# Optimization experiments

Hardware: AMD Instinct MI355X
Metric: run time of the kernel (lower is better)

Reference implementation:

```python
import jax, jax.numpy as jnp
import numpy as np
import math

B, T, D, DI, DFF, H = 4, 1024, 1024, 256, 4096, 16
S, N, E = 16, 256, 1024          # stat_num, token_num, exemplar_len
STAT_K, TOKEN_K = 8, 16
NEG = -1e6


def setup_inputs() -> dict:
    key = jax.random.key(0)
    ks = jax.random.split(key, 32)
    r = lambda i, shape: jax.random.normal(ks[i], shape, jnp.float32)
    w = lambda i, shape: r(i, shape) * 0.02
    return dict(
        x=r(0, (B, T, D)),
        stat_enc=r(1, (B * S, N, D)),
        exemplar_enc=r(2, (B, E, D)),
        stat_feature=r(3, (B, S, D)),
        intent_embed=r(4, (B, 1, DI)),
        Wq1=w(5, (D, D)), Wk1=w(6, (D, D)), Wv1=w(7, (D, D)), Wo1=w(8, (D, D)),
        Wq_stat=w(9, (D + DI, D)), Wq_token=w(10, (D + DI, D)),
        Wk_stat=w(11, (D, D)), Wk_token=w(12, (D, D)),
        Wv_sel=w(13, (D, D)), Wo_sel=w(14, (D, D)),
        Wq2=w(15, (D + DI, D)), Wk2=w(16, (D, D)), Wv2=w(17, (D, D)), Wo2=w(18, (D, D)),
        Wg=w(19, (2 * D, 1)),
        W1=w(20, (D, DFF)), b1=jnp.zeros((DFF,), jnp.float32),
        W2=w(21, (DFF, D)), b2=jnp.zeros((D,), jnp.float32),
        g1=jnp.ones((D,), jnp.float32), be1=jnp.zeros((D,), jnp.float32),
        g2=jnp.ones((D,), jnp.float32), be2=jnp.zeros((D,), jnp.float32),
        g3=jnp.ones((D,), jnp.float32), be3=jnp.zeros((D,), jnp.float32),
        stat_valid_len=jax.random.randint(ks[22], (B,), 1, S + 1),
        example_valid_len=jax.random.randint(ks[23], (B,), 1, E + 1),
    )


def _ln(x, g, b):
    m = x.mean(-1, keepdims=True)
    v = ((x - m) ** 2).mean(-1, keepdims=True)
    return (x - m) / jnp.sqrt(v + 1e-5) * g + b


def _mha(q, k, v, valid, Wq, Wk, Wv, Wo):
    Bq, Tq, _ = q.shape
    Sk = k.shape[1]
    sp = lambda z: z.reshape(Bq, z.shape[1], H, -1).transpose(0, 2, 1, 3)  # B,H,L,dh
    qh, kh, vh = sp(q @ Wq), sp(k @ Wk), sp(v @ Wv)
    dh = qh.shape[-1]
    sc = jnp.einsum('bhtd,bhsd->bhts', qh, kh) / math.sqrt(dh)
    vl = valid[:, None, None, None] if valid.ndim == 1 else valid[:, None, :, None]
    sc = jnp.where(jnp.arange(Sk)[None, None, None, :] < vl, sc, NEG)
    w = jax.nn.softmax(sc, axis=-1)
    out = jnp.einsum('bhts,bhsd->bhtd', w, vh).transpose(0, 2, 1, 3).reshape(Bq, Tq, -1)
    return out @ Wo


def _scatter_topk(scores, k):
    # keep top-k per row, everything else -> NEG (matches torch topk+scatter)
    shp = scores.shape
    flat = scores.reshape(-1, shp[-1])
    vals, idx = jax.lax.top_k(flat, k)
    out = jnp.full_like(flat, NEG).at[jnp.arange(flat.shape[0])[:, None], idx].set(vals)
    return out.reshape(shp)


def reference(x, stat_enc, exemplar_enc, stat_feature, intent_embed,
              Wq1, Wk1, Wv1, Wo1,
              Wq_stat, Wq_token, Wk_stat, Wk_token, Wv_sel, Wo_sel,
              Wq2, Wk2, Wv2, Wo2, Wg,
              W1, b1, W2, b2,
              g1, be1, g2, be2, g3, be3,
              stat_valid_len, example_valid_len):
    # masked self-attention (training mode -> causal valid lens)
    dec_valid = jnp.broadcast_to(jnp.arange(1, T + 1)[None, :], (B, T))
    x2 = _mha(x, x, x, dec_valid, Wq1, Wk1, Wv1, Wo1)
    y = _ln(x + x2, g1, be1)
    yi = jnp.concatenate([y, jnp.broadcast_to(intent_embed, (B, T, DI))], axis=-1)

    # selective hierarchical top-k attention
    qs = yi @ Wq_stat                      # [B,T,D]
    qt = yi @ Wq_token                     # [B,T,D]
    ks = stat_feature @ Wk_stat            # [B,S,D]
    kt = (stat_enc @ Wk_token).reshape(B, S, N, D)
    vv = (stat_enc @ Wv_sel).reshape(B, S, N, D)
    scale = math.sqrt(D)
    ssc = jnp.einsum('btd,bsd->bts', qs, ks) / scale
    ssc = jnp.where(jnp.arange(S)[None, None, :] < stat_valid_len[:, None, None], ssc, NEG)
    sw = jax.nn.softmax(_scatter_topk(ssc, min(S - 1, STAT_K)), axis=-1)   # [B,T,S]
    tsc = jnp.einsum('btd,bsnd->btsn', qt, kt) / scale                      # [B,T,S,N]
    tw = jax.nn.softmax(_scatter_topk(tsc, min(N - 1, TOKEN_K)), axis=-1)
    comb = sw[..., None] * tw                                               # [B,T,S,N]
    y2s = jnp.einsum('btsn,bsnd->btd', comb, vv) @ Wo_sel

    # exemplar cross-attention
    y2e = _mha(yi, exemplar_enc, exemplar_enc, example_valid_len, Wq2, Wk2, Wv2, Wo2)

    gate = jax.nn.sigmoid(jnp.concatenate([y2s, y2e], axis=-1) @ Wg)
    y2 = gate * y2s + (1.0 - gate) * y2e
    z = _ln(y + 2.0 * y2, g2, be2)
    ffn = jax.nn.relu(z @ W1 + b1) @ W2 + b2
    return _ln(z + ffn, g3, be3)
```

## Files before the change

kernel.cpp:

```cpp
#include <hip/hip_runtime.h>

typedef unsigned short u16;
typedef short s16x8 __attribute__((ext_vector_type(8)));
typedef u16 u16x4 __attribute__((ext_vector_type(4)));
typedef float f32x4 __attribute__((ext_vector_type(4)));

#define T_N   1024
#define NEGV  -1e6f
#define MB    (1L << 20)

__device__ __forceinline__ u16 f2bf(float f) {
    unsigned u = __float_as_uint(f);
    u += 0x7fffu + ((u >> 16) & 1u);
    return (u16)(u >> 16);
}
__device__ __forceinline__ float bf2f(u16 h) {
    return __uint_as_float(((unsigned)h) << 16);
}
__device__ __forceinline__ f32x4 mfma16(s16x8 a, s16x8 b, f32x4 c) {
    return __builtin_amdgcn_mfma_f32_16x16x32_bf16(a, b, c, 0, 0, 0);
}
__device__ __forceinline__ void gll16(const u16* g, u16* l) {
    __builtin_amdgcn_global_load_lds((const __attribute__((address_space(1))) void*)g,
                                     (__attribute__((address_space(3))) void*)l, 16, 0, 0);
}

struct P6 { const float* s[6]; u16* d[6]; };

__global__ __launch_bounds__(256) void transpose_cast_batch(P6 pp, int K, int N) {
    const float* __restrict__ src = pp.s[blockIdx.z];
    u16* __restrict__ dst = pp.d[blockIdx.z];
    __shared__ float tile[32][33];
    int nb = blockIdx.x * 32, kb = blockIdx.y * 32;
    int tx = threadIdx.x & 31, ty = threadIdx.x >> 5;
    #pragma unroll
    for (int i = 0; i < 4; i++)
        tile[ty + 8*i][tx] = src[(long)(kb + ty + 8*i) * N + nb + tx];
    __syncthreads();
    #pragma unroll
    for (int i = 0; i < 4; i++)
        dst[(long)(nb + ty + 8*i) * K + kb + tx] = f2bf(tile[tx][ty + 8*i]);
}

__global__ __launch_bounds__(256) void cast_bf16_kernel(const float* __restrict__ src,
                                                        u16* __restrict__ dst, long n) {
    long i = ((long)blockIdx.x * 256 + threadIdx.x) * 4;
    if (i >= n) return;
    float4 v = *(const float4*)(src + i);
    u16x4 o = { f2bf(v.x), f2bf(v.y), f2bf(v.z), f2bf(v.w) };
    *(u16x4*)(dst + i) = o;
}

template<typename OutT, bool RELU, bool HAS_BIAS>
__global__ __launch_bounds__(256) void gemm_bt(
    const u16* __restrict__ A, const u16* __restrict__ Bt, OutT* __restrict__ C,
    const float* __restrict__ bias, int M, int N, int K,
    int lda, int ldb, int ldc,
    int batchDivA, long sA, long sB, long sC)
{
    A  += (long)(blockIdx.z / batchDivA) * sA;
    Bt += (long)blockIdx.z * sB;
    C  += (long)blockIdx.z * sC;
    __shared__ __align__(16) u16 As[4096];
    __shared__ __align__(16) u16 Bs[4096];
    const int tid = threadIdx.x;
    const int wave = tid >> 6, lane = tid & 63;
    const int quad = lane >> 4, l16 = lane & 15;
    const int wr = (wave >> 1) * 64, wc = (wave & 1) * 64;
    const long row0 = (long)blockIdx.y * 128, col0 = (long)blockIdx.x * 128;

    f32x4 acc[4][4] = {};

    const int l4r = lane >> 2;
    const int l4c = (lane & 3) * 8;
    const int ra = wave * 32 + l4r;
    const u16* Ap0 = A + (row0 + ra) * (long)lda + l4c;
    const u16* Ap1 = Ap0 + 16L * lda;
    const u16* Bp0 = Bt + (col0 + ra) * (long)ldb + l4c;
    const u16* Bp1 = Bp0 + 16L * ldb;
    u16* AsW0 = &As[(wave * 32) * 32];
    u16* AsW1 = &As[(wave * 32 + 16) * 32];
    u16* BsW0 = &Bs[(wave * 32) * 32];
    u16* BsW1 = &Bs[(wave * 32 + 16) * 32];
    const bool aok0 = (row0 + wave * 32) < M;
    const bool aok1 = (row0 + wave * 32 + 16) < M;

    for (int k0 = 0; k0 < K; k0 += 32) {
        __syncthreads();
        if (aok0) gll16(Ap0 + k0, AsW0);
        if (aok1) gll16(Ap1 + k0, AsW1);
        gll16(Bp0 + k0, BsW0);
        gll16(Bp1 + k0, BsW1);
        __syncthreads();
        s16x8 af[4], bfr[4];
        #pragma unroll
        for (int i = 0; i < 4; i++)
            af[i]  = *(const s16x8*)&As[(wr + i*16 + l16) * 32 + quad*8];
        #pragma unroll
        for (int j = 0; j < 4; j++)
            bfr[j] = *(const s16x8*)&Bs[(wc + j*16 + l16) * 32 + quad*8];
        #pragma unroll
        for (int i = 0; i < 4; i++)
            #pragma unroll
            for (int j = 0; j < 4; j++)
                acc[i][j] = mfma16(af[i], bfr[j], acc[i][j]);
    }

    #pragma unroll
    for (int i = 0; i < 4; i++) {
        long row = row0 + wr + i*16 + quad*4;
        #pragma unroll
        for (int j = 0; j < 4; j++) {
            long col = col0 + wc + j*16 + l16;
            float bv = 0.f;
            if constexpr (HAS_BIAS) bv = bias[col];
            #pragma unroll
            for (int r = 0; r < 4; r++) {
                if (row + r < M) {
                    float v = acc[i][j][r] + bv;
                    if constexpr (RELU) v = fmaxf(v, 0.f);
                    if constexpr (sizeof(OutT) == 2) C[(row + r) * (long)ldc + col] = f2bf(v);
                    else                             C[(row + r) * (long)ldc + col] = v;
                }
            }
        }
    }
}

template<bool CAUSAL>
__global__ __launch_bounds__(256) void flash_attn_kernel(
    const u16* __restrict__ Q, const u16* __restrict__ Kg, const u16* __restrict__ Vg,
    const int* __restrict__ valid_len, u16* __restrict__ O,
    int qld, int kld, int vld)
{
    const int h = blockIdx.y, b = blockIdx.z;
    const int qt0 = blockIdx.x * 64;
    const int tid = threadIdx.x;
    const int wave = tid >> 6, lane = tid & 63;
    const int quad = lane >> 4, l16 = lane & 15;

    __shared__ __align__(16) u16 Qs[64][72];
    __shared__ __align__(16) u16 Ks[64][72];
    __shared__ __align__(16) u16 Vt[64][72];
    __shared__ __align__(16) u16 Ps[4][16][72];

    const int sr = tid >> 2, scc = (tid & 3) * 16;
    {
        const u16* qp = Q + ((long)b * T_N + qt0 + sr) * qld + h * 64 + scc;
        *(s16x8*)&Qs[sr][scc]     = *(const s16x8*)qp;
        *(s16x8*)&Qs[sr][scc + 8] = *(const s16x8*)(qp + 8);
    }
    float m_i[4] = {-1e30f, -1e30f, -1e30f, -1e30f};
    float l_i[4] = {0.f, 0.f, 0.f, 0.f};
    f32x4 o_acc[4] = {};

    int vl = 0, kend;
    if (CAUSAL) kend = qt0 + 64;
    else { vl = valid_len[b]; kend = (vl + 63) & ~63; }

    for (int kv0 = 0; kv0 < kend; kv0 += 64) {
        __syncthreads();
        {
            const u16* kp = Kg + ((long)b * T_N + kv0 + sr) * kld + h * 64 + scc;
            *(s16x8*)&Ks[sr][scc]     = *(const s16x8*)kp;
            *(s16x8*)&Ks[sr][scc + 8] = *(const s16x8*)(kp + 8);
            const u16* vp = Vg + ((long)b * T_N + kv0 + sr) * vld + h * 64 + scc;
            s16x8 v0 = *(const s16x8*)vp;
            s16x8 v1 = *(const s16x8*)(vp + 8);
            #pragma unroll
            for (int j = 0; j < 8; j++) {
                Vt[scc + j][sr]     = (u16)v0[j];
                Vt[scc + 8 + j][sr] = (u16)v1[j];
            }
        }
        __syncthreads();
        f32x4 sc[4] = {};
        #pragma unroll
        for (int kk = 0; kk < 64; kk += 32) {
            s16x8 aq = *(const s16x8*)&Qs[wave*16 + l16][kk + quad*8];
            #pragma unroll
            for (int j = 0; j < 4; j++) {
                s16x8 bk = *(const s16x8*)&Ks[j*16 + l16][kk + quad*8];
                sc[j] = mfma16(aq, bk, sc[j]);
            }
        }
        const int qrow = qt0 + wave*16 + quad*4;
        #pragma unroll
        for (int j = 0; j < 4; j++) {
            int kcol = kv0 + j*16 + l16;
            #pragma unroll
            for (int r = 0; r < 4; r++) {
                float s = sc[j][r] * 0.125f;
                bool ok = CAUSAL ? (kcol <= qrow + r) : (kcol < vl);
                sc[j][r] = ok ? s : -1e30f;
            }
        }
        float alpha[4];
        #pragma unroll
        for (int r = 0; r < 4; r++) {
            float mx = fmaxf(fmaxf(sc[0][r], sc[1][r]), fmaxf(sc[2][r], sc[3][r]));
            #pragma unroll
            for (int d = 1; d < 16; d <<= 1) mx = fmaxf(mx, __shfl_xor(mx, d, 64));
            float mn = fmaxf(m_i[r], mx);
            alpha[r] = __expf(m_i[r] - mn);
            m_i[r] = mn;
        }
        float rsum[4] = {0.f, 0.f, 0.f, 0.f};
        #pragma unroll
        for (int j = 0; j < 4; j++)
            #pragma unroll
            for (int r = 0; r < 4; r++) {
                float pv = __expf(sc[j][r] - m_i[r]);
                sc[j][r] = pv;
                rsum[r] += pv;
            }
        #pragma unroll
        for (int r = 0; r < 4; r++) {
            #pragma unroll
            for (int d = 1; d < 16; d <<= 1) rsum[r] += __shfl_xor(rsum[r], d, 64);
            l_i[r] = l_i[r] * alpha[r] + rsum[r];
        }
        #pragma unroll
        for (int j = 0; j < 4; j++)
            #pragma unroll
            for (int r = 0; r < 4; r++)
                Ps[wave][quad*4 + r][j*16 + l16] = f2bf(sc[j][r]);
        #pragma unroll
        for (int j2 = 0; j2 < 4; j2++)
            #pragma unroll
            for (int r = 0; r < 4; r++)
                o_acc[j2][r] *= alpha[r];
        __syncthreads();
        #pragma unroll
        for (int kk = 0; kk < 64; kk += 32) {
            s16x8 ap = *(const s16x8*)&Ps[wave][l16][kk + quad*8];
            #pragma unroll
            for (int j2 = 0; j2 < 4; j2++) {
                s16x8 bv = *(const s16x8*)&Vt[j2*16 + l16][kk + quad*8];
                o_acc[j2] = mfma16(ap, bv, o_acc[j2]);
            }
        }
    }
    #pragma unroll
    for (int j2 = 0; j2 < 4; j2++) {
        #pragma unroll
        for (int r = 0; r < 4; r++) {
            float v = o_acc[j2][r] / l_i[r];
            long row = (long)b * T_N + qt0 + wave*16 + quad*4 + r;
            O[row * 1024 + h*64 + j2*16 + l16] = f2bf(v);
        }
    }
}

__global__ __launch_bounds__(256) void ssc_kernel(
    const u16* __restrict__ qs, const u16* __restrict__ ks,
    const int* __restrict__ svl, float* __restrict__ ssc, int qld)
{
    const int t = blockIdx.x, b = blockIdx.y;
    const int wave = threadIdx.x >> 6, lane = threadIdx.x & 63;
    const u16* qrow = qs + ((long)b * T_N + t) * qld + lane * 16;
    const int vl = svl[b];
    for (int s = wave; s < 16; s += 4) {
        const u16* krow = ks + ((long)b * 16 + s) * 1024 + lane * 16;
        float acc = 0.f;
        #pragma unroll
        for (int seg = 0; seg < 2; seg++) {
            s16x8 qv = *(const s16x8*)(qrow + seg*8);
            s16x8 kv = *(const s16x8*)(krow + seg*8);
            #pragma unroll
            for (int j = 0; j < 8; j++) acc += bf2f((u16)qv[j]) * bf2f((u16)kv[j]);
        }
        #pragma unroll
        for (int d = 1; d < 64; d <<= 1) acc += __shfl_xor(acc, d, 64);
        if (lane == 0)
            ssc[((long)b * T_N + t) * 16 + s] = (s < vl) ? acc * (1.f/32.f) : NEGV;
    }
}

__global__ __launch_bounds__(256) void select_combine_kernel(
    const float* __restrict__ ssc, const float* __restrict__ tsc,
    const u16* __restrict__ vv, u16* __restrict__ out, int t0, int vld)
{
    const int tl = blockIdx.x, b = blockIdx.y;
    const int tg = t0 + tl;
    const int tid = threadIdx.x;
    const int wave = tid >> 6, lane = tid & 63;
    __shared__ float coeff[128];
    __shared__ long  rowoff[128];
    __shared__ int   sel_s[8];
    __shared__ float sel_w[8];

    if (wave == 0) {
        float cur = (lane < 16) ? ssc[((long)b * T_N + tg) * 16 + lane] : -3e38f;
        float mx0 = 0.f, ssum = 0.f, myv = -3e38f;
        int myi = 0;
        #pragma unroll
        for (int it = 0; it < 8; it++) {
            float mv = cur; int mi = lane;
            #pragma unroll
            for (int d = 1; d < 64; d <<= 1) {
                float ov = __shfl_xor(mv, d, 64);
                int   oi = __shfl_xor(mi, d, 64);
                if (ov > mv || (ov == mv && oi < mi)) { mv = ov; mi = oi; }
            }
            if (it == 0) mx0 = mv;
            ssum += __expf(mv - mx0);
            if (lane == it) { myv = mv; myi = mi; }
            if (lane == mi) cur = -3e38f;
        }
        if (lane < 8) { sel_s[lane] = myi; sel_w[lane] = __expf(myv - mx0) / ssum; }
    }
    __syncthreads();

    for (int slot = wave; slot < 8; slot += 4) {
        int s = sel_s[slot];
        float sw = sel_w[slot];
        const float* trow = tsc + (((long)b * 16 + s) * 512 + tl) * 256;
        float4 lv4 = *(const float4*)(trow + lane * 4);
        float loc[4] = { lv4.x, lv4.y, lv4.z, lv4.w };
        float mx0 = 0.f, tsum = 0.f, myv = -3e38f;
        int myi = 0;
        for (int it = 0; it < 16; it++) {
            float mv = -3e38f; int mi = 0;
            #pragma unroll
            for (int u = 0; u < 4; u++)
                if (loc[u] > mv) { mv = loc[u]; mi = lane*4 + u; }
            #pragma unroll
            for (int d = 1; d < 64; d <<= 1) {
                float ov = __shfl_xor(mv, d, 64);
                int   oi = __shfl_xor(mi, d, 64);
                if (ov > mv || (ov == mv && oi < mi)) { mv = ov; mi = oi; }
            }
            if (it == 0) mx0 = mv * (1.f/32.f);
            tsum += __expf(mv * (1.f/32.f) - mx0);
            if (lane == it) { myv = mv; myi = mi; }
            if ((mi >> 2) == lane) {
                int u = mi & 3;
                if (u == 0) loc[0] = -3e38f;
                else if (u == 1) loc[1] = -3e38f;
                else if (u == 2) loc[2] = -3e38f;
                else loc[3] = -3e38f;
            }
        }
        if (lane < 16) {
            coeff[slot * 16 + lane]  = sw * __expf(myv * (1.f/32.f) - mx0) / tsum;
            rowoff[slot * 16 + lane] = (long)((b * 16 + s) * 256 + myi) * vld;
        }
    }
    __syncthreads();

    const int d0 = tid * 4;
    float a0 = 0.f, a1 = 0.f, a2 = 0.f, a3 = 0.f;
    for (int r = 0; r < 128; r++) {
        float c = coeff[r];
        const u16* vp = vv + rowoff[r] + d0;
        u16x4 v4 = *(const u16x4*)vp;
        a0 += c * bf2f(v4[0]);
        a1 += c * bf2f(v4[1]);
        a2 += c * bf2f(v4[2]);
        a3 += c * bf2f(v4[3]);
    }
    u16x4 o4 = { f2bf(a0), f2bf(a1), f2bf(a2), f2bf(a3) };
    *(u16x4*)(out + ((long)b * T_N + tg) * 1024 + d0) = o4;
}

__device__ __forceinline__ float block_sum(float v, float* red) {
    #pragma unroll
    for (int d = 1; d < 64; d <<= 1) v += __shfl_xor(v, d, 64);
    __syncthreads();
    if ((threadIdx.x & 63) == 0) red[threadIdx.x >> 6] = v;
    __syncthreads();
    return red[0] + red[1] + red[2] + red[3];
}

__global__ __launch_bounds__(256) void ln1_kernel(
    const float* __restrict__ x, const float* __restrict__ x2,
    const float* __restrict__ intent, const float* __restrict__ g, const float* __restrict__ be,
    u16* __restrict__ yi)
{
    __shared__ float red[4];
    const long row = blockIdx.x;
    const int tid = threadIdx.x;
    const long base = row * 1024 + tid * 4;
    float4 xv = *(const float4*)(x + base);
    float4 dv = *(const float4*)(x2 + base);
    float h0 = xv.x + dv.x, h1 = xv.y + dv.y, h2 = xv.z + dv.z, h3 = xv.w + dv.w;
    float s1 = block_sum(h0 + h1 + h2 + h3, red);
    float s2 = block_sum(h0*h0 + h1*h1 + h2*h2 + h3*h3, red);
    float mean = s1 * (1.f/1024.f);
    float var = s2 * (1.f/1024.f) - mean * mean;
    float inv = rsqrtf(var + 1e-5f);
    const int c = tid * 4;
    float4 gv = *(const float4*)(g + c);
    float4 bv = *(const float4*)(be + c);
    float o0 = (h0 - mean) * inv * gv.x + bv.x;
    float o1 = (h1 - mean) * inv * gv.y + bv.y;
    float o2 = (h2 - mean) * inv * gv.z + bv.z;
    float o3 = (h3 - mean) * inv * gv.w + bv.w;
    u16x4 ob = { f2bf(o0), f2bf(o1), f2bf(o2), f2bf(o3) };
    *(u16x4*)(yi + row * 1280 + c) = ob;
    const int b = (int)(row >> 10);
    yi[row * 1280 + 1024 + tid] = f2bf(intent[b * 256 + tid]);
}

__global__ __launch_bounds__(256) void gate_ln2_kernel(
    const u16* __restrict__ yi, const float* __restrict__ y2s, const float* __restrict__ y2e,
    const float* __restrict__ Wg, const float* __restrict__ g, const float* __restrict__ be,
    float* __restrict__ z, u16* __restrict__ zbf)
{
    __shared__ float red[4];
    const long row = blockIdx.x;
    const int tid = threadIdx.x;
    const long base = row * 1024 + tid * 4;
    const int c = tid * 4;
    float4 sv = *(const float4*)(y2s + base);
    float4 ev = *(const float4*)(y2e + base);
    float4 w1 = *(const float4*)(Wg + c);
    float4 w2 = *(const float4*)(Wg + 1024 + c);
    float dot = sv.x*w1.x + sv.y*w1.y + sv.z*w1.z + sv.w*w1.w
              + ev.x*w2.x + ev.y*w2.y + ev.z*w2.z + ev.w*w2.w;
    float tot = block_sum(dot, red);
    float gate = 1.f / (1.f + __expf(-tot));
    u16x4 yv4 = *(const u16x4*)(yi + row * 1280 + c);
    float h0 = bf2f(yv4[0]) + 2.f * (gate * sv.x + (1.f - gate) * ev.x);
    float h1 = bf2f(yv4[1]) + 2.f * (gate * sv.y + (1.f - gate) * ev.y);
    float h2 = bf2f(yv4[2]) + 2.f * (gate * sv.z + (1.f - gate) * ev.z);
    float h3 = bf2f(yv4[3]) + 2.f * (gate * sv.w + (1.f - gate) * ev.w);
    float s1 = block_sum(h0 + h1 + h2 + h3, red);
    float s2 = block_sum(h0*h0 + h1*h1 + h2*h2 + h3*h3, red);
    float mean = s1 * (1.f/1024.f);
    float var = s2 * (1.f/1024.f) - mean * mean;
    float inv = rsqrtf(var + 1e-5f);
    float4 gv = *(const float4*)(g + c);
    float4 bv = *(const float4*)(be + c);
    float o0 = (h0 - mean) * inv * gv.x + bv.x;
    float o1 = (h1 - mean) * inv * gv.y + bv.y;
    float o2 = (h2 - mean) * inv * gv.z + bv.z;
    float o3 = (h3 - mean) * inv * gv.w + bv.w;
    *(float4*)(z + base) = make_float4(o0, o1, o2, o3);
    u16x4 ob = { f2bf(o0), f2bf(o1), f2bf(o2), f2bf(o3) };
    *(u16x4*)(zbf + row * 1024 + c) = ob;
}

__global__ __launch_bounds__(256) void ln3_kernel(
    const float* __restrict__ z, const float* __restrict__ p0, const float* __restrict__ p1,
    const float* __restrict__ b2,
    const float* __restrict__ g, const float* __restrict__ be, float* __restrict__ out)
{
    __shared__ float red[4];
    const long row = blockIdx.x;
    const int tid = threadIdx.x;
    const long base = row * 1024 + tid * 4;
    const int c = tid * 4;
    float4 zv = *(const float4*)(z + base);
    float4 f0 = *(const float4*)(p0 + base);
    float4 f1 = *(const float4*)(p1 + base);
    float4 bb = *(const float4*)(b2 + c);
    float h0 = zv.x + f0.x + f1.x + bb.x;
    float h1 = zv.y + f0.y + f1.y + bb.y;
    float h2 = zv.z + f0.z + f1.z + bb.z;
    float h3 = zv.w + f0.w + f1.w + bb.w;
    float s1 = block_sum(h0 + h1 + h2 + h3, red);
    float s2 = block_sum(h0*h0 + h1*h1 + h2*h2 + h3*h3, red);
    float mean = s1 * (1.f/1024.f);
    float var = s2 * (1.f/1024.f) - mean * mean;
    float inv = rsqrtf(var + 1e-5f);
    float4 gv = *(const float4*)(g + c);
    float4 bv = *(const float4*)(be + c);
    float o0 = (h0 - mean) * inv * gv.x + bv.x;
    float o1 = (h1 - mean) * inv * gv.y + bv.y;
    float o2 = (h2 - mean) * inv * gv.z + bv.z;
    float o3 = (h3 - mean) * inv * gv.w + bv.w;
    *(float4*)(out + base) = make_float4(o0, o1, o2, o3);
}

extern "C" void kernel_launch(void* const* d_in, const int* in_sizes, int n_in,
                              void* d_out, int out_size, void* d_ws, size_t ws_size,
                              hipStream_t stream)
{
    (void)in_sizes; (void)n_in; (void)out_size; (void)ws_size;
    const float* x      = (const float*)d_in[0];
    const float* stat_e = (const float*)d_in[1];
    const float* exem   = (const float*)d_in[2];
    const float* sfeat  = (const float*)d_in[3];
    const float* intent = (const float*)d_in[4];
    const float* Wg  = (const float*)d_in[19];
    const float* b1  = (const float*)d_in[21];
    const float* b2  = (const float*)d_in[23];
    const float* g1  = (const float*)d_in[24]; const float* be1 = (const float*)d_in[25];
    const float* g2  = (const float*)d_in[26]; const float* be2 = (const float*)d_in[27];
    const float* g3  = (const float*)d_in[28]; const float* be3 = (const float*)d_in[29];
    const int* svl = (const int*)d_in[30];
    const int* evl = (const int*)d_in[31];
    float* outp = (float*)d_out;

    char* base = (char*)d_ws;
    u16*  bufA  = (u16*)(base + 0*MB);
    u16*  qkv1  = (u16*)(base + 8*MB);
    float* x2a  = (float*)(base + 8*MB);
    u16*  kv2   = (u16*)(base + 8*MB);
    u16*  w1t   = (u16*)(base + 8*MB);
    u16*  w2t   = (u16*)(base + 16*MB);
    u16*  yibf  = (u16*)(base + 32*MB);
    u16*  buf3  = (u16*)(base + 42*MB);
    u16*  zbf   = (u16*)(base + 42*MB);
    u16*  sebf  = (u16*)(base + 66*MB);
    float* tsch = (float*)(base + 66*MB);
    u16*  hid   = (u16*)(base + 66*MB);
    u16*  ktvv  = (u16*)(base + 98*MB);
    float* y2sf = (float*)(base + 98*MB);
    float* p0f  = (float*)(base + 98*MB);
    u16*  exbf  = (u16*)(base + 114*MB);
    float* y2ef = (float*)(base + 122*MB);
    float* zf   = (float*)(base + 138*MB);
    u16*  sfbf  = (u16*)(base + 162*MB);
    u16*  ksbf  = (u16*)(base + 162*MB + 256*1024);
    float* sscf = (float*)(base + 162*MB + 512*1024);
    char* wpool = base + 163*MB;

    dim3 blk(256);
    auto cast = [&](const float* s, u16* d, long n) {
        cast_bf16_kernel<<<dim3((unsigned)((n/4 + 255) / 256)), blk, 0, stream>>>(s, d, n);
    };
    auto g_n = [&](const u16* A, const u16* Bt, u16* C, int M, int N, int K,
                   int lda, int ldb, int ldc) {
        gemm_bt<u16,false,false><<<dim3(N/128, (M+127)/128, 1), blk, 0, stream>>>(
            A, Bt, C, nullptr, M, N, K, lda, ldb, ldc, 1, 0, 0, 0);
    };
    auto g_f = [&](const u16* A, const u16* Bt, float* C, int M, int N, int K,
                   int lda, int ldb, int ldc) {
        gemm_bt<float,false,false><<<dim3(N/128, (M+127)/128, 1), blk, 0, stream>>>(
            A, Bt, C, nullptr, M, N, K, lda, ldb, ldc, 1, 0, 0, 0);
    };

    u16* wqkv1t = (u16*)wpool;
    u16* wo1t   = (u16*)(wpool) + 3L*1024*1024;
    {
        P6 pp{};
        pp.s[0]=(const float*)d_in[5]; pp.d[0]=wqkv1t;
        pp.s[1]=(const float*)d_in[6]; pp.d[1]=wqkv1t + 1L*1024*1024;
        pp.s[2]=(const float*)d_in[7]; pp.d[2]=wqkv1t + 2L*1024*1024;
        pp.s[3]=(const float*)d_in[8]; pp.d[3]=wo1t;
        transpose_cast_batch<<<dim3(32, 32, 4), blk, 0, stream>>>(pp, 1024, 1024);
    }
    cast(x, bufA, 4096L*1024);
    g_n(bufA, wqkv1t, qkv1, 4096, 3072, 1024, 1024, 1024, 3072);
    flash_attn_kernel<true><<<dim3(16, 16, 4), blk, 0, stream>>>(
        qkv1, qkv1 + 1024, qkv1 + 2048, nullptr, bufA, 3072, 3072, 3072);
    g_f(bufA, wo1t, x2a, 4096, 1024, 1024, 1024, 1024, 1024);
    ln1_kernel<<<dim3(4096), blk, 0, stream>>>(x, x2a, intent, g1, be1, yibf);

    u16* wq3t = (u16*)wpool;
    {
        P6 pp{};
        pp.s[0]=(const float*)d_in[9];  pp.d[0]=wq3t;
        pp.s[1]=(const float*)d_in[10]; pp.d[1]=wq3t + 1L*1024*1280;
        pp.s[2]=(const float*)d_in[15]; pp.d[2]=wq3t + 2L*1024*1280;
        transpose_cast_batch<<<dim3(32, 40, 3), blk, 0, stream>>>(pp, 1280, 1024);
    }
    g_n(yibf, wq3t, buf3, 4096, 3072, 1280, 1280, 1280, 3072);
    u16* wkst = (u16*)wpool;
    u16* wkv  = (u16*)(wpool) + 1L*1024*1024;
    {
        P6 pp{};
        pp.s[0]=(const float*)d_in[11]; pp.d[0]=wkst;
        pp.s[1]=(const float*)d_in[12]; pp.d[1]=wkv;
        pp.s[2]=(const float*)d_in[13]; pp.d[2]=wkv + 1L*1024*1024;
        transpose_cast_batch<<<dim3(32, 32, 3), blk, 0, stream>>>(pp, 1024, 1024);
    }
    cast(sfeat, sfbf, 64L*1024);
    cast(stat_e, sebf, 16384L*1024);
    g_n(sfbf, wkst, ksbf, 64, 1024, 1024, 1024, 1024, 1024);
    g_n(sebf, wkv, ktvv, 16384, 2048, 1024, 1024, 1024, 2048);
    ssc_kernel<<<dim3(1024, 4), blk, 0, stream>>>(buf3, ksbf, svl, sscf, 3072);
    for (int hh = 0; hh < 2; hh++) {
        long t0 = hh * 512;
        gemm_bt<float,false,false><<<dim3(2, 4, 64), blk, 0, stream>>>(
            buf3 + 1024 + t0*3072, ktvv, tsch, nullptr, 512, 256, 1024,
            3072, 2048, 256, 16, (long)T_N*3072, 256L*2048, 512L*256);
        select_combine_kernel<<<dim3(512, 4), blk, 0, stream>>>(
            sscf, tsch, ktvv + 1024, bufA, (int)t0, 2048);
    }
    u16* wost = (u16*)wpool;
    u16* wkv2 = (u16*)(wpool) + 1L*1024*1024;
    u16* wo2t = (u16*)(wpool) + 3L*1024*1024;
    {
        P6 pp{};
        pp.s[0]=(const float*)d_in[14]; pp.d[0]=wost;
        pp.s[1]=(const float*)d_in[16]; pp.d[1]=wkv2;
        pp.s[2]=(const float*)d_in[17]; pp.d[2]=wkv2 + 1L*1024*1024;
        pp.s[3]=(const float*)d_in[18]; pp.d[3]=wo2t;
        transpose_cast_batch<<<dim3(32, 32, 4), blk, 0, stream>>>(pp, 1024, 1024);
    }
    g_f(bufA, wost, y2sf, 4096, 1024, 1024, 1024, 1024, 1024);

    cast(exem, exbf, 4096L*1024);
    g_n(exbf, wkv2, kv2, 4096, 2048, 1024, 1024, 1024, 2048);
    flash_attn_kernel<false><<<dim3(16, 16, 4), blk, 0, stream>>>(
        buf3 + 2048, kv2, kv2 + 1024, evl, bufA, 3072, 2048, 2048);
    g_f(bufA, wo2t, y2ef, 4096, 1024, 1024, 1024, 1024, 1024);

    gate_ln2_kernel<<<dim3(4096), blk, 0, stream>>>(yibf, y2sf, y2ef, Wg, g2, be2, zf, zbf);

    {
        P6 pp{}; pp.s[0] = (const float*)d_in[20]; pp.d[0] = w1t;
        transpose_cast_batch<<<dim3(128, 32, 1), blk, 0, stream>>>(pp, 1024, 4096);
    }
    {
        P6 pp{}; pp.s[0] = (const float*)d_in[22]; pp.d[0] = w2t;
        transpose_cast_batch<<<dim3(32, 128, 1), blk, 0, stream>>>(pp, 4096, 1024);
    }
    gemm_bt<u16,true,true><<<dim3(32, 32, 1), blk, 0, stream>>>(
        zbf, w1t, hid, b1, 4096, 4096, 1024, 1024, 1024, 4096, 1, 0, 0, 0);
    gemm_bt<float,false,false><<<dim3(8, 32, 2), blk, 0, stream>>>(
        hid, w2t, p0f, nullptr, 4096, 1024, 2048, 4096, 4096, 1024,
        1, 2048, 2048, 4096L*1024);

    ln3_kernel<<<dim3(4096), blk, 0, stream>>>(zf, p0f, p0f + 4096L*1024, b2, g3, be3, outp);
}
```

Measured before the change: 1.031 ms.

## Add 256x256-tile 8-wave GEMM with 4-stage LDS pipeline for large GEMMs

Adds a new GEMM kernel with 256x256 output tiles and 512 threads per block. It uses a four-buffer global_load_lds prefetch pipeline that splits A and B staging across two MFMA phases, and raises wave priority around the MFMA blocks. Most of the large projection and FFN GEMMs move to it, which cuts global/L2 traffic per FLOP and raises arithmetic intensity. In exchange the tile grids are coarser, so some launches have few blocks (for example 128 blocks for the token-score GEMM). The new kernel has no M-boundary guards and needs LDS swizzle-free reads, which can cause bank conflicts.

```diff
diff --git a/kernel.cpp b/kernel.cpp
--- a/kernel.cpp
+++ b/kernel.cpp
@@ -122,6 +122,120 @@
                     if constexpr (sizeof(OutT) == 2) C[(row + r) * (long)ldc + col] = f2bf(v);
                     else                             C[(row + r) * (long)ldc + col] = v;
                 }
+            }
+        }
+    }
+}
+
+template<typename OutT, bool RELU, bool HAS_BIAS>
+__global__ __launch_bounds__(512, 2) void gemm_bt256(
+    const u16* __restrict__ A, const u16* __restrict__ Bt, OutT* __restrict__ C,
+    const float* __restrict__ bias, int M, int N, int K,
+    int lda, int ldb, int ldc,
+    int batchDivA, long sA, long sB, long sC)
+{
+    A  += (long)(blockIdx.z / batchDivA) * sA;
+    Bt += (long)blockIdx.z * sB;
+    C  += (long)blockIdx.z * sC;
+    __shared__ __align__(16) u16 As[4][8192];
+    __shared__ __align__(16) u16 Bs[4][8192];
+    const int tid = threadIdx.x;
+    const int wave = tid >> 6, lane = tid & 63;
+    const int quad = lane >> 4, l16 = lane & 15;
+    const int wm = wave >> 2, wn = wave & 3;
+    const long row0 = (long)blockIdx.y * 256, col0 = (long)blockIdx.x * 256;
+
+    const int srow = tid >> 2;
+    const int scol = (tid & 3) * 8;
+    const u16* Ag = A  + (row0 + srow) * (long)lda + scol;
+    const u16* Bg = Bt + (col0 + srow) * (long)ldb + scol;
+    const int ldsoff = wave * 512;
+
+    f32x4 acc[8][4] = {};
+    const int NT = K >> 5;
+
+    auto stageA = [&](int kt, int buf) {
+        gll16(Ag + (long)kt * 32,            &As[buf][ldsoff]);
+        gll16(Ag + (long)kt * 32 + 128L*lda, &As[buf][4096 + ldsoff]);
+    };
+    auto stageB = [&](int kt, int buf) {
+        gll16(Bg + (long)kt * 32,            &Bs[buf][ldsoff]);
+        gll16(Bg + (long)kt * 32 + 128L*ldb, &Bs[buf][4096 + ldsoff]);
+    };
+
+    stageA(0, 0); stageB(0, 0);
+    stageA(1, 1); stageB(1, 1);
+    stageA(2, 2); stageB(2, 2);
+    asm volatile("s_waitcnt vmcnt(8)" ::: "memory");
+    __builtin_amdgcn_s_barrier();
+
+    const int arow = wm * 128 + l16;
+    const int brow = wn * 64  + l16;
+    const int kq   = quad * 8;
+
+    for (int kt = 0; kt < NT; ++kt) {
+        const int b  = kt & 3;
+        const int sb = (kt + 3) & 3;
+        const bool st = (kt + 3) < NT;
+        const u16* Ab = As[b];
+        const u16* Bb = Bs[b];
+
+        s16x8 bfr[4], af[4];
+        #pragma unroll
+        for (int j = 0; j < 4; ++j)
+            bfr[j] = *(const s16x8*)&Bb[(brow + j*16) * 32 + kq];
+        #pragma unroll
+        for (int i = 0; i < 4; ++i)
+            af[i] = *(const s16x8*)&Ab[(arow + i*16) * 32 + kq];
+        if (st) stageA(kt + 3, sb);
+        __builtin_amdgcn_s_barrier();
+        asm volatile("s_waitcnt lgkmcnt(0)" ::: "memory");
+        __builtin_amdgcn_sched_barrier(0);
+        __builtin_amdgcn_s_setprio(1);
+        #pragma unroll
+        for (int i = 0; i < 4; ++i)
+            #pragma unroll
+            for (int j = 0; j < 4; ++j)
+                acc[i][j] = mfma16(af[i], bfr[j], acc[i][j]);
+        __builtin_amdgcn_s_setprio(0);
+        __builtin_amdgcn_s_barrier();
+
+        #pragma unroll
+        for (int i = 0; i < 4; ++i)
+            af[i] = *(const s16x8*)&Ab[(arow + (i + 4)*16) * 32 + kq];
+        if (st) stageB(kt + 3, sb);
+        __builtin_amdgcn_s_barrier();
+        asm volatile("s_waitcnt lgkmcnt(0)" ::: "memory");
+        __builtin_amdgcn_sched_barrier(0);
+        __builtin_amdgcn_s_setprio(1);
+        #pragma unroll
+        for (int i = 0; i < 4; ++i)
+            #pragma unroll
+            for (int j = 0; j < 4; ++j)
+                acc[i + 4][j] = mfma16(af[i], bfr[j], acc[i + 4][j]);
+        __builtin_amdgcn_s_setprio(0);
+
+        const int rem = NT - 2 - kt;
+        if (rem >= 2)      asm volatile("s_waitcnt vmcnt(8)" ::: "memory");
+        else if (rem == 1) asm volatile("s_waitcnt vmcnt(4)" ::: "memory");
+        else if (rem == 0) asm volatile("s_waitcnt vmcnt(0)" ::: "memory");
+        __builtin_amdgcn_s_barrier();
+    }
+
+    #pragma unroll
+    for (int i = 0; i < 8; ++i) {
+        const long row = row0 + wm*128 + i*16 + quad*4;
+        #pragma unroll
+        for (int j = 0; j < 4; ++j) {
+            const long col = col0 + wn*64 + j*16 + l16;
+            float bv = 0.f;
+            if constexpr (HAS_BIAS) bv = bias[col];
+            #pragma unroll
+            for (int r = 0; r < 4; ++r) {
+                float v = acc[i][j][r] + bv;
+                if constexpr (RELU) v = fmaxf(v, 0.f);
+                if constexpr (sizeof(OutT) == 2) C[(row + r) * (long)ldc + col] = f2bf(v);
+                else                             C[(row + r) * (long)ldc + col] = v;
             }
         }
     }
@@ -519,6 +633,7 @@
     char* wpool = base + 163*MB;
 
     dim3 blk(256);
+    dim3 blk512(512);
     auto cast = [&](const float* s, u16* d, long n) {
         cast_bf16_kernel<<<dim3((unsigned)((n/4 + 255) / 256)), blk, 0, stream>>>(s, d, n);
     };
@@ -532,6 +647,11 @@
         gemm_bt<float,false,false><<<dim3(N/128, (M+127)/128, 1), blk, 0, stream>>>(
             A, Bt, C, nullptr, M, N, K, lda, ldb, ldc, 1, 0, 0, 0);
     };
+    auto g256_n = [&](const u16* A, const u16* Bt, u16* C, int M, int N, int K,
+                      int lda, int ldb, int ldc) {
+        gemm_bt256<u16,false,false><<<dim3(N/256, M/256, 1), blk512, 0, stream>>>(
+            A, Bt, C, nullptr, M, N, K, lda, ldb, ldc, 1, 0, 0, 0);
+    };
 
     u16* wqkv1t = (u16*)wpool;
     u16* wo1t   = (u16*)(wpool) + 3L*1024*1024;
@@ -544,7 +664,7 @@
         transpose_cast_batch<<<dim3(32, 32, 4), blk, 0, stream>>>(pp, 1024, 1024);
     }
     cast(x, bufA, 4096L*1024);
-    g_n(bufA, wqkv1t, qkv1, 4096, 3072, 1024, 1024, 1024, 3072);
+    g256_n(bufA, wqkv1t, qkv1, 4096, 3072, 1024, 1024, 1024, 3072);
     flash_attn_kernel<true><<<dim3(16, 16, 4), blk, 0, stream>>>(
         qkv1, qkv1 + 1024, qkv1 + 2048, nullptr, bufA, 3072, 3072, 3072);
     g_f(bufA, wo1t, x2a, 4096, 1024, 1024, 1024, 1024, 1024);
@@ -558,7 +678,7 @@
         pp.s[2]=(const float*)d_in[15]; pp.d[2]=wq3t + 2L*1024*1280;
         transpose_cast_batch<<<dim3(32, 40, 3), blk, 0, stream>>>(pp, 1280, 1024);
     }
-    g_n(yibf, wq3t, buf3, 4096, 3072, 1280, 1280, 1280, 3072);
+    g256_n(yibf, wq3t, buf3, 4096, 3072, 1280, 1280, 1280, 3072);
     u16* wkst = (u16*)wpool;
     u16* wkv  = (u16*)(wpool) + 1L*1024*1024;
     {
@@ -571,11 +691,11 @@
     cast(sfeat, sfbf, 64L*1024);
     cast(stat_e, sebf, 16384L*1024);
     g_n(sfbf, wkst, ksbf, 64, 1024, 1024, 1024, 1024, 1024);
-    g_n(sebf, wkv, ktvv, 16384, 2048, 1024, 1024, 1024, 2048);
+    g256_n(sebf, wkv, ktvv, 16384, 2048, 1024, 1024, 1024, 2048);
     ssc_kernel<<<dim3(1024, 4), blk, 0, stream>>>(buf3, ksbf, svl, sscf, 3072);
     for (int hh = 0; hh < 2; hh++) {
         long t0 = hh * 512;
-        gemm_bt<float,false,false><<<dim3(2, 4, 64), blk, 0, stream>>>(
+        gemm_bt256<float,false,false><<<dim3(1, 2, 64), blk512, 0, stream>>>(
             buf3 + 1024 + t0*3072, ktvv, tsch, nullptr, 512, 256, 1024,
             3072, 2048, 256, 16, (long)T_N*3072, 256L*2048, 512L*256);
         select_combine_kernel<<<dim3(512, 4), blk, 0, stream>>>(
@@ -595,7 +715,7 @@
     g_f(bufA, wost, y2sf, 4096, 1024, 1024, 1024, 1024, 1024);
 
     cast(exem, exbf, 4096L*1024);
-    g_n(exbf, wkv2, kv2, 4096, 2048, 1024, 1024, 1024, 2048);
+    g256_n(exbf, wkv2, kv2, 4096, 2048, 1024, 1024, 1024, 2048);
     flash_attn_kernel<false><<<dim3(16, 16, 4), blk, 0, stream>>>(
         buf3 + 2048, kv2, kv2 + 1024, evl, bufA, 3072, 2048, 2048);
     g_f(bufA, wo2t, y2ef, 4096, 1024, 1024, 1024, 1024, 1024);
@@ -610,9 +730,9 @@
         P6 pp{}; pp.s[0] = (const float*)d_in[22]; pp.d[0] = w2t;
         transpose_cast_batch<<<dim3(32, 128, 1), blk, 0, stream>>>(pp, 4096, 1024);
     }
-    gemm_bt<u16,true,true><<<dim3(32, 32, 1), blk, 0, stream>>>(
+    gemm_bt256<u16,true,true><<<dim3(16, 16, 1), blk512, 0, stream>>>(
         zbf, w1t, hid, b1, 4096, 4096, 1024, 1024, 1024, 4096, 1, 0, 0, 0);
-    gemm_bt<float,false,false><<<dim3(8, 32, 2), blk, 0, stream>>>(
+    gemm_bt256<float,false,false><<<dim3(4, 16, 2), blk512, 0, stream>>>(
         hid, w2t, p0f, nullptr, 4096, 1024, 2048, 4096, 4096, 1024,
         1, 2048, 2048, 4096L*1024);
 
```

After: 1.059 ms. +2.8%, slower.
